# Optimization experiments

Hardware: AMD Instinct MI355X
Metric: run time of the kernel (lower is better)

## Reference

```python
import jax, jax.numpy as jnp
import numpy as np

D_MODEL = 1024
NUM_HEADS = 16
B, S = 1, 4096


def setup_inputs() -> dict:
    key = jax.random.key(0)
    kx, kq, kk, kv, ko = jax.random.split(key, 5)
    std = (1.0 / D_MODEL) ** 0.5
    def trunc(k):
        return std * jax.random.truncated_normal(k, -3.0, 3.0, (D_MODEL, D_MODEL), dtype=jnp.float32)
    return {
        "x": jax.random.normal(kx, (B, S, D_MODEL), dtype=jnp.float32),
        "W_Q": trunc(kq),
        "W_K": trunc(kk),
        "W_V": trunc(kv),
        "W_O": trunc(ko),
    }


def reference(x, W_Q, W_K, W_V, W_O):
    Bx, Sx, Dm = x.shape
    H = NUM_HEADS
    d_attn = Dm // H
    # projections (torch code uses x @ W.T)
    Q = x @ W_Q.T
    K = x @ W_K.T
    V = x @ W_V.T
    # [B, H, S, d]
    Q = Q.reshape(Bx, Sx, H, d_attn).transpose(0, 2, 1, 3)
    K = K.reshape(Bx, Sx, H, d_attn).transpose(0, 2, 1, 3)
    V = V.reshape(Bx, Sx, H, d_attn).transpose(0, 2, 1, 3)
    scale = 1.0 / jnp.sqrt(jnp.asarray(d_attn, dtype=x.dtype))
    # [B, H, S, S] scores
    attn = jnp.einsum("bhqd,bhkd->bhqk", Q, K) * scale
    causal = jnp.tril(jnp.ones((Sx, Sx), dtype=bool))
    attn = jnp.where(causal, attn, jnp.asarray(-jnp.inf, dtype=attn.dtype))
    probs = jax.nn.softmax(attn, axis=-1)
    y = jnp.einsum("bhqk,bhkd->bhqd", probs, V)
    y = y.transpose(0, 2, 1, 3).reshape(Bx, Sx, Dm)
    return y @ W_O.T
```

## Files before the change

### kernel.cpp

```cpp
#include <hip/hip_runtime.h>

#define S_LEN 4096
#define DMODEL 1024
#define NHEADS 16

typedef __attribute__((ext_vector_type(8))) short bf16x8;
typedef __attribute__((ext_vector_type(4))) float f32x4;
typedef unsigned short u16;
typedef unsigned int u32;
typedef unsigned long long u64;

#define MEMFENCE asm volatile("" ::: "memory")

__device__ inline u16 f2bf(float f) {
    union { float f; u32 u; } v; v.f = f;
    u32 r = v.u + 0x7fffu + ((v.u >> 16) & 1u);
    return (u16)(r >> 16);
}

__device__ inline u32 pkbf2(float a, float b) {
    union { float f; u32 u; } ua, ub; ua.f = a; ub.f = b;
    const u32 ra = ua.u + 0x7fffu + ((ua.u >> 16) & 1u);
    const u32 rb = ub.u + 0x7fffu + ((ub.u >> 16) & 1u);
    return __builtin_amdgcn_perm(rb, ra, 0x07060302u);
}

__device__ inline u32 pkbf2f(float a, float b) {
    union { float f; u32 u; } ua, ub; ua.f = a; ub.f = b;
    const u32 ra = ua.u + 0x8000u;
    const u32 rb = ub.u + 0x8000u;
    return __builtin_amdgcn_perm(rb, ra, 0x07060302u);
}

__device__ inline void cp16(const void* g, void* l) {
    __builtin_amdgcn_global_load_lds(
        (const __attribute__((address_space(1))) unsigned int*)g,
        (__attribute__((address_space(3))) unsigned int*)l, 16, 0, 0);
}

__global__ __launch_bounds__(256) void cvt_all(const float* __restrict__ x,
                                               const float* __restrict__ wq,
                                               const float* __restrict__ wk,
                                               const float* __restrict__ wv,
                                               const float* __restrict__ wo,
                                               u16* __restrict__ xb,
                                               u16* __restrict__ w3,
                                               u16* __restrict__ wob) {
    const int b = blockIdx.x;
    const float* s; u16* d; int off;
    const int NW = DMODEL * DMODEL;
    if (b < 2048)      { s = x;  d = xb;          off = b * 2048; }
    else if (b < 2560) { s = wq; d = w3;          off = (b - 2048) * 2048; }
    else if (b < 3072) { s = wk; d = w3 + NW;     off = (b - 2560) * 2048; }
    else if (b < 3584) { s = wv; d = w3 + 2 * NW; off = (b - 3072) * 2048; }
    else               { s = wo; d = wob;         off = (b - 3584) * 2048; }
    const int i = off + threadIdx.x * 8;
    const float4 a = *(const float4*)(s + i);
    const float4 c = *(const float4*)(s + i + 4);
    u16 t[8];
    t[0] = f2bf(a.x); t[1] = f2bf(a.y); t[2] = f2bf(a.z); t[3] = f2bf(a.w);
    t[4] = f2bf(c.x); t[5] = f2bf(c.y); t[6] = f2bf(c.z); t[7] = f2bf(c.w);
    *(bf16x8*)(d + i) = *(const bf16x8*)t;
}

__global__ __launch_bounds__(256) void gemm_qkv(const u16* __restrict__ A,
                                                const u16* __restrict__ B3,
                                                u16* __restrict__ Qo,
                                                u16* __restrict__ Ko,
                                                u16* __restrict__ Vo) {
    __shared__ __align__(16) u16 As[3][128 * 32];
    __shared__ __align__(16) u16 Bs[3][128 * 32];
    const int tid = threadIdx.x, lane = tid & 63, wave = tid >> 6;
    const int wm = (wave >> 1) * 64, wn = (wave & 1) * 64;
    const int m0 = blockIdx.y * 128, n0 = blockIdx.x * 128;
    const int l15 = lane & 15, quad = lane >> 4;

    f32x4 acc[4][4];
#pragma unroll
    for (int i = 0; i < 4; i++)
#pragma unroll
        for (int j = 0; j < 4; j++) acc[i][j] = (f32x4){0.f, 0.f, 0.f, 0.f};

    const int r0 = tid >> 2, c0 = (tid & 3) * 8;

#define STAGE_QKV(buf, kkb)                                                        \
    {                                                                              \
        cp16(A + (size_t)(m0 + r0) * 1024 + (kkb) + c0,       As[buf] + r0 * 32 + c0); \
        cp16(A + (size_t)(m0 + r0 + 64) * 1024 + (kkb) + c0,  As[buf] + (r0 + 64) * 32 + c0); \
        cp16(B3 + (size_t)(n0 + r0) * 1024 + (kkb) + c0,      Bs[buf] + r0 * 32 + c0); \
        cp16(B3 + (size_t)(n0 + r0 + 64) * 1024 + (kkb) + c0, Bs[buf] + (r0 + 64) * 32 + c0); \
    }

#define COMPUTE_QKV(cur)                                                           \
    {                                                                              \
        bf16x8 af[4], bfr[4];                                                      \
        _Pragma("unroll")                                                          \
        for (int i = 0; i < 4; i++)                                                \
            af[i] = *(const bf16x8*)(As[cur] + (wm + i * 16 + l15) * 32 + quad * 8); \
        _Pragma("unroll")                                                          \
        for (int j = 0; j < 4; j++)                                                \
            bfr[j] = *(const bf16x8*)(Bs[cur] + (wn + j * 16 + l15) * 32 + quad * 8); \
        _Pragma("unroll")                                                          \
        for (int i = 0; i < 4; i++)                                                \
            _Pragma("unroll")                                                      \
            for (int j = 0; j < 4; j++)                                            \
                acc[i][j] = __builtin_amdgcn_mfma_f32_16x16x32_bf16(af[i], bfr[j], acc[i][j], 0, 0, 0); \
    }

    STAGE_QKV(0, 0);
    MEMFENCE;
    STAGE_QKV(1, 32);
    MEMFENCE;

    for (int ks = 0; ks < 31; ks++) {
        asm volatile("s_waitcnt vmcnt(4)" ::: "memory");
        __builtin_amdgcn_s_barrier();
        __builtin_amdgcn_sched_barrier(0);
        if (ks < 30) {
            STAGE_QKV((ks + 2) % 3, (ks + 2) * 32);
            MEMFENCE;
        }
        COMPUTE_QKV(ks % 3);
    }
    asm volatile("s_waitcnt vmcnt(0)" ::: "memory");
    __builtin_amdgcn_s_barrier();
    __builtin_amdgcn_sched_barrier(0);
    COMPUTE_QKV(1);
#undef STAGE_QKV
#undef COMPUTE_QKV

    const int which = n0 >> 10;
    const int n0r = n0 & 1023;
    u16* dst = (which == 0) ? Qo : (which == 1) ? Ko : Vo;
    if (which < 2) {
        const float sc = (which == 0) ? 0.125f * 1.4426950408889634f : 1.0f;
#pragma unroll
        for (int i = 0; i < 4; i++)
#pragma unroll
            for (int j = 0; j < 4; j++) {
                const int col = n0r + wn + j * 16 + l15;
                const int h = col >> 6, c = col & 63;
#pragma unroll
                for (int r = 0; r < 4; r++) {
                    const int row = m0 + wm + i * 16 + quad * 4 + r;
                    dst[(size_t)h * S_LEN * 64 + (size_t)row * 64 + c] = f2bf(acc[i][j][r] * sc);
                }
            }
    } else {
#pragma unroll
        for (int i = 0; i < 4; i++) {
            const int row0 = m0 + wm + i * 16 + quad * 4;
#pragma unroll
            for (int j = 0; j < 4; j++) {
                const int col = n0r + wn + j * 16 + l15;
                const int h = col >> 6, c = col & 63;
                const u32 y0 = pkbf2(acc[i][j][0], acc[i][j][1]);
                const u32 y1 = pkbf2(acc[i][j][2], acc[i][j][3]);
                *(u64*)(dst + (size_t)h * S_LEN * 64 + (size_t)c * S_LEN + row0) =
                    (u64)y0 | ((u64)y1 << 32);
            }
        }
    }
}

__global__ __launch_bounds__(256) void gemm_out(const u16* __restrict__ A,
                                                const u16* __restrict__ B,
                                                float* __restrict__ C) {
    __shared__ __align__(16) u16 As[2][64 * 64];
    __shared__ __align__(16) u16 Bs[2][128 * 64];
    const int tid = threadIdx.x, lane = tid & 63, wave = tid >> 6;
    const int wm = (wave >> 1) * 32, wn = (wave & 1) * 64;
    const int bx = blockIdx.x;
    const int n0 = (bx & 7) * 128, m0 = (bx >> 3) * 64;
    const int l15 = lane & 15, quad = lane >> 4;
    const int swz = l15 & 7;

    f32x4 acc[2][4];
#pragma unroll
    for (int i = 0; i < 2; i++)
#pragma unroll
        for (int j = 0; j < 4; j++) acc[i][j] = (f32x4){0.f, 0.f, 0.f, 0.f};

#define STAGE_OUT(buf, kb)                                                              \
    {                                                                                   \
        _Pragma("unroll")                                                               \
        for (int q = 0; q < 2; q++) {                                                   \
            const int ch = tid + q * 256;                                               \
            const int ar = ch >> 3, ac = ((ch & 7) ^ (ar & 7)) * 8;                     \
            cp16(A + (size_t)(m0 + ar) * 1024 + (kb) + ac, As[buf] + ch * 8);           \
        }                                                                               \
        _Pragma("unroll")                                                               \
        for (int q = 0; q < 4; q++) {                                                   \
            const int ch = tid + q * 256;                                               \
            const int br = ch >> 3, bc = ((ch & 7) ^ (br & 7)) * 8;                     \
            cp16(B + (size_t)(n0 + br) * 1024 + (kb) + bc, Bs[buf] + ch * 8);           \
        }                                                                               \
    }

    STAGE_OUT(0, 0);
    int cur = 0;
    for (int kk = 0; kk < 1024; kk += 64) {
        __syncthreads();
        if (kk + 64 < 1024) STAGE_OUT(cur ^ 1, kk + 64);
#pragma unroll
        for (int h = 0; h < 2; h++) {
            const int cc = (h * 4 + quad) ^ swz;
            bf16x8 af[2], bfr[4];
#pragma unroll
            for (int i = 0; i < 2; i++)
                af[i] = *(const bf16x8*)(As[cur] + (wm + i * 16 + l15) * 64 + cc * 8);
#pragma unroll
            for (int j = 0; j < 4; j++)
                bfr[j] = *(const bf16x8*)(Bs[cur] + (wn + j * 16 + l15) * 64 + cc * 8);
#pragma unroll
            for (int i = 0; i < 2; i++)
#pragma unroll
                for (int j = 0; j < 4; j++)
                    acc[i][j] = __builtin_amdgcn_mfma_f32_16x16x32_bf16(af[i], bfr[j], acc[i][j], 0, 0, 0);
        }
        cur ^= 1;
    }
#undef STAGE_OUT

#pragma unroll
    for (int i = 0; i < 2; i++)
#pragma unroll
        for (int j = 0; j < 4; j++)
#pragma unroll
            for (int r = 0; r < 4; r++) {
                const int row = m0 + wm + i * 16 + quad * 4 + r;
                const int col = n0 + wn + j * 16 + l15;
                C[(size_t)row * 1024 + col] = acc[i][j][r];
            }
}

__global__ __launch_bounds__(256, 3) void attn(const u16* __restrict__ Q,
                                               const u16* __restrict__ Kh,
                                               const u16* __restrict__ Vt,
                                               u16* __restrict__ Y) {
    __shared__ __align__(16) u16 KW[2][4][2048];
    __shared__ __align__(16) u16 VW[4][2048];
    const int b = blockIdx.x;
    const int head = b & 15;
    const int jq = 63 - (b >> 4);
    const int nkt = jq + 1;
    const int np = (nkt + 1) >> 1;
    const int qa = jq * 64;
    const int tid = threadIdx.x, lane = tid & 63, w = tid >> 6;
    const int l15 = lane & 15, quad = lane >> 4;
    const int swz = l15 & 7;

    const u16* Qp = Q + (size_t)head * S_LEN * 64;
    const u16* Kp = Kh + (size_t)head * S_LEN * 64;
    const u16* Vp = Vt + (size_t)head * 64 * S_LEN;

    bf16x8 qf[4][2];
#pragma unroll
    for (int qg = 0; qg < 4; qg++)
#pragma unroll
        for (int h = 0; h < 2; h++)
            qf[qg][h] = *(const bf16x8*)(Qp + (size_t)(qa + qg * 16 + l15) * 64 + h * 32 + quad * 8);
    MEMFENCE;

    f32x4 o[4][4];
#pragma unroll
    for (int dg = 0; dg < 4; dg++)
#pragma unroll
        for (int qg = 0; qg < 4; qg++) o[dg][qg] = (f32x4){0.f, 0.f, 0.f, 0.f};
    float lp[4] = {0.f, 0.f, 0.f, 0.f};

    const int keyl = w * 16 + quad * 4;
    const int s4 = (l15 >> 1) & 3;
    const int ceo = (((quad >> 1) ^ s4)) * 8 + (quad & 1) * 4;
    const int coo = ceo ^ 16;

    union PU { u32 d[4]; bf16x8 v; };
    union VU { u64 d[2]; bf16x8 v; };

#define STAGE_K(buf, kp2)                                                               \
    {                                                                                   \
        _Pragma("unroll")                                                               \
        for (int i = 0; i < 4; i++) {                                                   \
            const int gk = (kp2) * 128 + w * 16 + (i & 1) * 8 + (lane >> 3) + (i >> 1) * 64; \
            const int lc = (lane & 7) ^ (lane >> 3);                                    \
            cp16(Kp + (size_t)gk * 64 + lc * 8, KW[buf][w] + i * 512 + lane * 8);       \
        }                                                                               \
    }

#define STAGE_V(kp2)                                                                    \
    {                                                                                   \
        _Pragma("unroll")                                                               \
        for (int i = 0; i < 4; i++) {                                                   \
            const int d = i * 16 + (lane >> 2);                                         \
            const int L = (lane & 3) ^ ((lane >> 3) & 3);                               \
            const int s = (kp2) * 128 + w * 16 + (L >> 1) * 64 + (L & 1) * 8;           \
            cp16(Vp + (size_t)d * S_LEN + s, VW[w] + i * 512 + lane * 8);               \
        }                                                                               \
    }

#define QK_PHASE(DGE, DGO, HO)                                                          \
    {                                                                                   \
        const u16* Kb = KW[cur][w];                                                     \
        const bf16x8 kE0 = *(const bf16x8*)(Kb + l15 * 64 + (quad ^ swz) * 8);          \
        const bf16x8 kE1 = *(const bf16x8*)(Kb + l15 * 64 + ((4 ^ quad) ^ swz) * 8);    \
        const bf16x8 kO0 = *(const bf16x8*)(Kb + (16 + l15) * 64 + (quad ^ swz) * 8);   \
        const bf16x8 kO1 = *(const bf16x8*)(Kb + (16 + l15) * 64 + ((4 ^ quad) ^ swz) * 8); \
        __builtin_amdgcn_s_setprio(1);                                                  \
        _Pragma("unroll")                                                               \
        for (int qg = 0; qg < 4; qg++) {                                                \
            const int ql = qg * 16 + l15;                                               \
            f32x4 c = (f32x4){0.f, 0.f, 0.f, 0.f};                                      \
            c = __builtin_amdgcn_mfma_f32_16x16x32_bf16(kE0, qf[qg][0], c, 0, 0, 0);    \
            c = __builtin_amdgcn_mfma_f32_16x16x32_bf16(kE1, qf[qg][1], c, 0, 0, 0);    \
            float p0 = __builtin_amdgcn_exp2f(c[0]);                                    \
            float p1 = __builtin_amdgcn_exp2f(c[1]);                                    \
            float p2 = __builtin_amdgcn_exp2f(c[2]);                                    \
            float p3 = __builtin_amdgcn_exp2f(c[3]);                                    \
            if (DGE) {                                                                  \
                if (keyl + 0 > ql) p0 = 0.f;                                            \
                if (keyl + 1 > ql) p1 = 0.f;                                            \
                if (keyl + 2 > ql) p2 = 0.f;                                            \
                if (keyl + 3 > ql) p3 = 0.f;                                            \
            }                                                                           \
            lp[qg] += (p0 + p1) + (p2 + p3);                                            \
            pu[qg].d[0] = pkbf2f(p0, p1);                                               \
            pu[qg].d[1] = pkbf2f(p2, p3);                                               \
            if (HO) {                                                                   \
                f32x4 cc = (f32x4){0.f, 0.f, 0.f, 0.f};                                 \
                cc = __builtin_amdgcn_mfma_f32_16x16x32_bf16(kO0, qf[qg][0], cc, 0, 0, 0); \
                cc = __builtin_amdgcn_mfma_f32_16x16x32_bf16(kO1, qf[qg][1], cc, 0, 0, 0); \
                float q0 = __builtin_amdgcn_exp2f(cc[0]);                               \
                float q1 = __builtin_amdgcn_exp2f(cc[1]);                               \
                float q2 = __builtin_amdgcn_exp2f(cc[2]);                               \
                float q3 = __builtin_amdgcn_exp2f(cc[3]);                               \
                if (DGO) {                                                              \
                    if (keyl + 0 > ql) q0 = 0.f;                                        \
                    if (keyl + 1 > ql) q1 = 0.f;                                        \
                    if (keyl + 2 > ql) q2 = 0.f;                                        \
                    if (keyl + 3 > ql) q3 = 0.f;                                        \
                }                                                                       \
                lp[qg] += (q0 + q1) + (q2 + q3);                                        \
                pu[qg].d[2] = pkbf2f(q0, q1);                                           \
                pu[qg].d[3] = pkbf2f(q2, q3);                                           \
            } else {                                                                    \
                pu[qg].d[2] = 0u; pu[qg].d[3] = 0u;                                     \
            }                                                                           \
        }                                                                               \
        __builtin_amdgcn_s_setprio(0);                                                  \
    }

#define PV_PHASE()                                                                      \
    {                                                                                   \
        __builtin_amdgcn_s_setprio(1);                                                  \
        _Pragma("unroll")                                                               \
        for (int dg = 0; dg < 4; dg++) {                                                \
            const u16* vb = VW[w] + (dg * 16 + l15) * 32;                               \
            VU vf;                                                                      \
            vf.d[0] = *(const u64*)(vb + ceo);                                          \
            vf.d[1] = *(const u64*)(vb + coo);                                          \
            _Pragma("unroll")                                                           \
            for (int qg = 0; qg < 4; qg++)                                              \
                o[dg][qg] = __builtin_amdgcn_mfma_f32_16x16x32_bf16(vf.v, pu[qg].v, o[dg][qg], 0, 0, 0); \
        }                                                                               \
        __builtin_amdgcn_s_setprio(0);                                                  \
    }

    STAGE_K(0, 0);
    MEMFENCE;
    STAGE_V(0);
    MEMFENCE;

    int cur = 0;
    for (int kp = 0; kp < np - 1; kp++) {
        STAGE_K(cur ^ 1, kp + 1);
        asm volatile("s_waitcnt vmcnt(8)" ::: "memory");
        __builtin_amdgcn_sched_barrier(0);
        PU pu[4];
        QK_PHASE(false, false, true);
        asm volatile("s_waitcnt vmcnt(4)" ::: "memory");
        __builtin_amdgcn_sched_barrier(0);
        PV_PHASE();
        MEMFENCE;
        STAGE_V(kp + 1);
        MEMFENCE;
        cur ^= 1;
    }
    {
        asm volatile("s_waitcnt vmcnt(4)" ::: "memory");
        __builtin_amdgcn_sched_barrier(0);
        const bool dE = !(jq & 1);
        const bool hO = (jq & 1);
        PU pu[4];
        QK_PHASE(dE, true, hO);
        asm volatile("s_waitcnt vmcnt(0)" ::: "memory");
        __builtin_amdgcn_sched_barrier(0);
        PV_PHASE();
    }
#undef STAGE_K
#undef STAGE_V
#undef QK_PHASE
#undef PV_PHASE

    float* OR = (float*)&KW[0][0][0];
    float* LR = (float*)((char*)&KW[0][0][0] + 24576);
#pragma unroll
    for (int qg = 0; qg < 4; qg++) {
        lp[qg] += __shfl_xor(lp[qg], 16);
        lp[qg] += __shfl_xor(lp[qg], 32);
    }
    __syncthreads();
    if (lane < 16) {
#pragma unroll
        for (int qg = 0; qg < 4; qg++) LR[(w * 4 + qg) * 16 + lane] = lp[qg];
    }
    const int qrow = tid >> 2;
    const int qgr = qrow >> 4, lq = qrow & 15;
    const int dpart = (tid & 3) * 4;
    __syncthreads();
    const float lsum = LR[qgr * 16 + lq] + LR[(4 + qgr) * 16 + lq] +
                       LR[(8 + qgr) * 16 + lq] + LR[(12 + qgr) * 16 + lq];
    const float inv = 1.f / lsum;
#pragma unroll
    for (int dg = 0; dg < 4; dg++) {
        if (dg) __syncthreads();
#pragma unroll
        for (int qg = 0; qg < 4; qg++)
            *(f32x4*)&OR[((w * 4 + qg) * 16 + l15) * 20 + quad * 4] = o[dg][qg];
        __syncthreads();
        f32x4 s = (f32x4){0.f, 0.f, 0.f, 0.f};
#pragma unroll
        for (int sw = 0; sw < 4; sw++)
            s += *(const f32x4*)&OR[((sw * 4 + qgr) * 16 + lq) * 20 + dpart];
        const u32 y0 = pkbf2(s[0] * inv, s[1] * inv);
        const u32 y1 = pkbf2(s[2] * inv, s[3] * inv);
        *(u64*)(Y + (size_t)(qa + qrow) * DMODEL + head * 64 + dg * 16 + dpart) =
            (u64)y0 | ((u64)y1 << 32);
    }
}

extern "C" void kernel_launch(void* const* d_in, const int* in_sizes, int n_in,
                              void* d_out, int out_size, void* d_ws, size_t ws_size,
                              hipStream_t stream) {
    const float* x  = (const float*)d_in[0];
    const float* wq = (const float*)d_in[1];
    const float* wk = (const float*)d_in[2];
    const float* wv = (const float*)d_in[3];
    const float* wo = (const float*)d_in[4];
    float* out = (float*)d_out;

    u16* qh  = (u16*)d_ws;
    u16* kh  = qh + (size_t)S_LEN * DMODEL;
    u16* vt  = kh + (size_t)S_LEN * DMODEL;
    u16* xb  = vt + (size_t)S_LEN * DMODEL;
    u16* y   = xb;
    u16* wb3 = xb + (size_t)S_LEN * DMODEL;
    u16* wob = wb3 + (size_t)3 * DMODEL * DMODEL;

    const dim3 blk(256);

    cvt_all<<<4096, blk, 0, stream>>>(x, wq, wk, wv, wo, xb, wb3, wob);
    gemm_qkv<<<dim3(3 * DMODEL / 128, S_LEN / 128), blk, 0, stream>>>(xb, wb3, qh, kh, vt);
    attn<<<1024, blk, 0, stream>>>(qh, kh, vt, y);
    gemm_out<<<512, blk, 0, stream>>>(y, wob, out);
}
```

Baseline: 204.0 us.

## Load V fragments directly from global into registers, dropping V LDS staging

The attention kernel no longer stages V tiles into shared memory through async copies. Each lane now loads its V fragments straight from global memory into registers with 8-byte loads, and the vmcnt waits are adjusted to match. This frees LDS and drops the LDS read traffic for V, and the launch bound is raised to allow four blocks per CU. The trade-off is uncoalesced 8-byte global loads, more registers held live across the QK phase, and possible spilling under the tighter register budget.

```diff
diff --git a/kernel.cpp b/kernel.cpp
--- a/kernel.cpp
+++ b/kernel.cpp
@@ -234,12 +234,11 @@
             }
 }
 
-__global__ __launch_bounds__(256, 3) void attn(const u16* __restrict__ Q,
+__global__ __launch_bounds__(256, 4) void attn(const u16* __restrict__ Q,
                                                const u16* __restrict__ Kh,
                                                const u16* __restrict__ Vt,
                                                u16* __restrict__ Y) {
     __shared__ __align__(16) u16 KW[2][4][2048];
-    __shared__ __align__(16) u16 VW[4][2048];
     const int b = blockIdx.x;
     const int head = b & 15;
     const int jq = 63 - (b >> 4);
@@ -270,9 +269,11 @@
     float lp[4] = {0.f, 0.f, 0.f, 0.f};
 
     const int keyl = w * 16 + quad * 4;
-    const int s4 = (l15 >> 1) & 3;
-    const int ceo = (((quad >> 1) ^ s4)) * 8 + (quad & 1) * 4;
-    const int coo = ceo ^ 16;
+
+    const u16* vp0 = Vp + (size_t)l15 * S_LEN + w * 16 + quad * 4;
+    const u16* vp1 = vp0 + (size_t)16 * S_LEN;
+    const u16* vp2 = vp0 + (size_t)32 * S_LEN;
+    const u16* vp3 = vp0 + (size_t)48 * S_LEN;
 
     union PU { u32 d[4]; bf16x8 v; };
     union VU { u64 d[2]; bf16x8 v; };
@@ -287,16 +288,11 @@
         }                                                                               \
     }
 
-#define STAGE_V(kp2)                                                                    \
-    {                                                                                   \
-        _Pragma("unroll")                                                               \
-        for (int i = 0; i < 4; i++) {                                                   \
-            const int d = i * 16 + (lane >> 2);                                         \
-            const int L = (lane & 3) ^ ((lane >> 3) & 3);                               \
-            const int s = (kp2) * 128 + w * 16 + (L >> 1) * 64 + (L & 1) * 8;           \
-            cp16(Vp + (size_t)d * S_LEN + s, VW[w] + i * 512 + lane * 8);               \
-        }                                                                               \
-    }
+#define LOAD_V(V0, V1, V2, V3)                                                          \
+    V0.d[0] = *(const u64*)(vp0); V0.d[1] = *(const u64*)(vp0 + 64); vp0 += 128;        \
+    V1.d[0] = *(const u64*)(vp1); V1.d[1] = *(const u64*)(vp1 + 64); vp1 += 128;        \
+    V2.d[0] = *(const u64*)(vp2); V2.d[1] = *(const u64*)(vp2 + 64); vp2 += 128;        \
+    V3.d[0] = *(const u64*)(vp3); V3.d[1] = *(const u64*)(vp3 + 64); vp3 += 128;
 
 #define QK_PHASE(DGE, DGO, HO)                                                          \
     {                                                                                   \
@@ -349,44 +345,48 @@
         __builtin_amdgcn_s_setprio(0);                                                  \
     }
 
-#define PV_PHASE()                                                                      \
+#define PV_PHASE(V0, V1, V2, V3)                                                        \
     {                                                                                   \
         __builtin_amdgcn_s_setprio(1);                                                  \
         _Pragma("unroll")                                                               \
-        for (int dg = 0; dg < 4; dg++) {                                                \
-            const u16* vb = VW[w] + (dg * 16 + l15) * 32;                               \
-            VU vf;                                                                      \
-            vf.d[0] = *(const u64*)(vb + ceo);                                          \
-            vf.d[1] = *(const u64*)(vb + coo);                                          \
-            _Pragma("unroll")                                                           \
-            for (int qg = 0; qg < 4; qg++)                                              \
-                o[dg][qg] = __builtin_amdgcn_mfma_f32_16x16x32_bf16(vf.v, pu[qg].v, o[dg][qg], 0, 0, 0); \
-        }                                                                               \
+        for (int qg = 0; qg < 4; qg++)                                                  \
+            o[0][qg] = __builtin_amdgcn_mfma_f32_16x16x32_bf16(V0.v, pu[qg].v, o[0][qg], 0, 0, 0); \
+        _Pragma("unroll")                                                               \
+        for (int qg = 0; qg < 4; qg++)                                                  \
+            o[1][qg] = __builtin_amdgcn_mfma_f32_16x16x32_bf16(V1.v, pu[qg].v, o[1][qg], 0, 0, 0); \
+        _Pragma("unroll")                                                               \
+        for (int qg = 0; qg < 4; qg++)                                                  \
+            o[2][qg] = __builtin_amdgcn_mfma_f32_16x16x32_bf16(V2.v, pu[qg].v, o[2][qg], 0, 0, 0); \
+        _Pragma("unroll")                                                               \
+        for (int qg = 0; qg < 4; qg++)                                                  \
+            o[3][qg] = __builtin_amdgcn_mfma_f32_16x16x32_bf16(V3.v, pu[qg].v, o[3][qg], 0, 0, 0); \
         __builtin_amdgcn_s_setprio(0);                                                  \
     }
 
     STAGE_K(0, 0);
-    MEMFENCE;
-    STAGE_V(0);
     MEMFENCE;
 
     int cur = 0;
     for (int kp = 0; kp < np - 1; kp++) {
         STAGE_K(cur ^ 1, kp + 1);
-        asm volatile("s_waitcnt vmcnt(8)" ::: "memory");
+        MEMFENCE;
+        VU v0, v1, v2, v3;
+        LOAD_V(v0, v1, v2, v3);
+        MEMFENCE;
+        asm volatile("s_waitcnt vmcnt(12)" ::: "memory");
         __builtin_amdgcn_sched_barrier(0);
         PU pu[4];
         QK_PHASE(false, false, true);
         asm volatile("s_waitcnt vmcnt(4)" ::: "memory");
         __builtin_amdgcn_sched_barrier(0);
-        PV_PHASE();
+        PV_PHASE(v0, v1, v2, v3);
+        cur ^= 1;
+    }
+    {
+        VU v0, v1, v2, v3;
+        LOAD_V(v0, v1, v2, v3);
         MEMFENCE;
-        STAGE_V(kp + 1);
-        MEMFENCE;
-        cur ^= 1;
-    }
-    {
-        asm volatile("s_waitcnt vmcnt(4)" ::: "memory");
+        asm volatile("s_waitcnt vmcnt(8)" ::: "memory");
         __builtin_amdgcn_sched_barrier(0);
         const bool dE = !(jq & 1);
         const bool hO = (jq & 1);
@@ -394,10 +394,10 @@
         QK_PHASE(dE, true, hO);
         asm volatile("s_waitcnt vmcnt(0)" ::: "memory");
         __builtin_amdgcn_sched_barrier(0);
-        PV_PHASE();
+        PV_PHASE(v0, v1, v2, v3);
     }
 #undef STAGE_K
-#undef STAGE_V
+#undef LOAD_V
 #undef QK_PHASE
 #undef PV_PHASE
 
```

Result: slower. 422.8 us (+107.3%).
